# Optimization experiments

Measured on AMD Instinct MI355X. Metric: run time of the kernel, lower is better.

Reference implementation:

```python
import jax, jax.numpy as jnp
import numpy as np

N = 40000      # num atoms
E = 640000     # num edges (avg degree 16)
H = 128        # hidden_channels
R = 64         # num_rbf
NB = 3         # num interaction blocks
CUT = 5.0      # cutoff_upper
NT = 100       # num atom types (embedding rows)


def setup_inputs() -> dict:
    key = jax.random.key(0)
    ks = jax.random.split(key, 24)

    def lin_w(k, fan_in, fan_out):
        # xavier-uniform-like scale
        lim = np.sqrt(6.0 / (fan_in + fan_out)).astype(np.float32)
        return jax.random.uniform(k, (fan_in, fan_out), jnp.float32, -lim, lim)

    def stack_w(k, fan_in, fan_out):
        kk = jax.random.split(k, NB)
        return jnp.stack([lin_w(kk[i], fan_in, fan_out) for i in range(NB)])

    inp = {}
    inp["atom_types"] = jax.random.randint(ks[0], (N,), 0, NT)
    inp["edge_index"] = jax.random.randint(ks[1], (2, E), 0, N)
    inp["edge_weight"] = jax.random.uniform(ks[2], (E,), jnp.float32) * CUT

    inp["emb"] = jax.random.normal(ks[3], (NT, H), jnp.float32) * 0.1
    # CFConv params per block (stacked on leading NB axis)
    inp["lin1_w"] = stack_w(ks[4], H, H)            # no bias
    inp["fw1"] = stack_w(ks[5], R, H)
    inp["fb1"] = jnp.zeros((NB, H), jnp.float32)
    inp["fw2"] = stack_w(ks[6], H, H)
    inp["fb2"] = jnp.zeros((NB, H), jnp.float32)
    inp["lin2_w"] = stack_w(ks[7], H, H)
    inp["lin2_b"] = jnp.zeros((NB, H), jnp.float32)
    # InteractionBlock trailing linear
    inp["lin_w"] = stack_w(ks[8], H, H)
    inp["lin_b"] = jnp.zeros((NB, H), jnp.float32)
    # output network: H -> H//2 -> 1
    inp["o1_w"] = lin_w(ks[9], H, H // 2)
    inp["o1_b"] = jnp.zeros((H // 2,), jnp.float32)
    inp["o2_w"] = lin_w(ks[10], H // 2, 1)
    inp["o2_b"] = jnp.zeros((1,), jnp.float32)
    return inp


def _schnet_fwd(atom_types, edge_index, edge_weight, emb, lin1_w, fw1, fb1,
                fw2, fb2, lin2_w, lin2_b, lin_w, lin_b, o1_w, o1_b, o2_w, o2_b):
    # Gaussian RBF expansion of distances: (E, R)
    offsets = jnp.linspace(0.0, CUT, R).astype(edge_weight.dtype)
    coeff = -0.5 / (offsets[1] - offsets[0]) ** 2
    rbf = jnp.exp(coeff * (edge_weight[:, None] - offsets[None, :]) ** 2)
    # cosine cutoff envelope: (E,)
    C = 0.5 * (jnp.cos(jnp.pi * edge_weight / CUT) + 1.0)
    C = C * (edge_weight < CUT).astype(edge_weight.dtype)

    src = edge_index[0]
    dst = edge_index[1]

    x = emb[atom_types]  # (N, H)
    for b in range(NB):
        # filter network on expanded distances: (E, H)
        W = jnp.tanh(rbf @ fw1[b] + fb1[b]) @ fw2[b] + fb2[b]
        W = W * C[:, None]
        # CFConv: project, gather by src, modulate, scatter-sum to dst
        h = x @ lin1_w[b]                              # (N, H)
        msg = h[src] * W                               # (E, H)
        agg = jax.ops.segment_sum(msg, dst, num_segments=N)  # (N, H)
        y = agg @ lin2_w[b] + lin2_b[b]
        # InteractionBlock tail: activation then linear; residual in SchNet
        y = jnp.tanh(y) @ lin_w[b] + lin_b[b]
        x = x + y
    # output network: per-atom scalar energies (N, 1)
    energy = jnp.tanh(x @ o1_w + o1_b) @ o2_w + o2_b
    return energy


def reference(atom_types, edge_index, edge_weight, emb, lin1_w, fw1, fb1,
              fw2, fb2, lin2_w, lin2_b, lin_w, lin_b, o1_w, o1_b, o2_w, o2_b):
    return _schnet_fwd(atom_types, edge_index, edge_weight, emb, lin1_w, fw1,
                       fb1, fw2, fb2, lin2_w, lin2_b, lin_w, lin_b, o1_w,
                       o1_b, o2_w, o2_b)
```

## Files before the change

### kernel.cpp

```cpp
#include <hip/hip_runtime.h>
#include <math.h>

#define N_ATOMS 40000
#define E_EDGES 640000
#define H 128
#define RBF 64
#define NBLK 3
#define CUTF 5.0f
#define TBL 4096

__device__ __forceinline__ float fast_tanh(float x) {
    return 1.0f - 2.0f / (1.0f + __expf(2.0f * x));
}

__global__ __launch_bounds__(128) void k_embw(const float* __restrict__ emb,
                                              const float* __restrict__ lin1,
                                              float* __restrict__ embw) {
    const int t = blockIdx.x;
    const int c = threadIdx.x;
    float s = 0.0f;
#pragma unroll 8
    for (int k = 0; k < H; ++k) s = fmaf(emb[t * H + k], lin1[(size_t)k * H + c], s);
    embw[t * H + c] = s;
}

__global__ __launch_bounds__(256) void k_embed2(const int* __restrict__ types,
                                                const float* __restrict__ emb,
                                                const float* __restrict__ embw,
                                                float* __restrict__ x,
                                                float* __restrict__ h) {
    int flat4 = blockIdx.x * 256 + threadIdx.x;
    int i = flat4 >> 5;
    int c4 = flat4 & 31;
    int t = types[i];
    ((float4*)(x + (size_t)i * H))[c4] = ((const float4*)(emb + (size_t)t * H))[c4];
    ((float4*)(h + (size_t)i * H))[c4] = ((const float4*)(embw + (size_t)t * H))[c4];
}

__global__ __launch_bounds__(256) void k_count(const int* __restrict__ eidx,
                                               int* __restrict__ cnt) {
    int e = blockIdx.x * 256 + threadIdx.x;
    atomicAdd(&cnt[eidx[E_EDGES + e]], 1);
}

__global__ __launch_bounds__(1024) void k_scanA(const int* __restrict__ cnt,
                                                int* __restrict__ bsum) {
    __shared__ int ws[16];
    const int tid = threadIdx.x, lane = tid & 63, wid = tid >> 6;
    int idx = blockIdx.x * 1024 + tid;
    int v = (idx < N_ATOMS) ? cnt[idx] : 0;
#pragma unroll
    for (int off = 32; off; off >>= 1) v += __shfl_xor(v, off, 64);
    if (lane == 0) ws[wid] = v;
    __syncthreads();
    if (tid == 0) {
        int s = 0;
#pragma unroll
        for (int w = 0; w < 16; ++w) s += ws[w];
        bsum[blockIdx.x] = s;
    }
}

__global__ __launch_bounds__(64) void k_scanB(const int* __restrict__ bsum,
                                              int* __restrict__ boff) {
    const int lane = threadIdx.x;
    int v = (lane < 40) ? bsum[lane] : 0;
    int inc = v;
#pragma unroll
    for (int off = 1; off < 64; off <<= 1) {
        int t = __shfl_up(inc, off, 64);
        if (lane >= off) inc += t;
    }
    if (lane < 40) boff[lane] = inc - v;
}

__global__ __launch_bounds__(1024) void k_scanC(const int* __restrict__ cnt,
                                                const int* __restrict__ boff,
                                                int* __restrict__ cursor,
                                                int* __restrict__ rstart) {
    __shared__ int wsum[16];
    __shared__ int woff[16];
    const int tid = threadIdx.x, lane = tid & 63, wid = tid >> 6;
    int idx = blockIdx.x * 1024 + tid;
    int v = (idx < N_ATOMS) ? cnt[idx] : 0;
    int inc = v;
#pragma unroll
    for (int off = 1; off < 64; off <<= 1) {
        int t = __shfl_up(inc, off, 64);
        if (lane >= off) inc += t;
    }
    if (lane == 63) wsum[wid] = inc;
    __syncthreads();
    if (tid == 0) {
        int acc = 0;
#pragma unroll
        for (int w = 0; w < 16; ++w) { woff[w] = acc; acc += wsum[w]; }
    }
    __syncthreads();
    if (idx < N_ATOMS) {
        int ex = boff[blockIdx.x] + woff[wid] + inc - v;
        cursor[idx] = ex;
        rstart[idx] = ex;
    }
}

__global__ __launch_bounds__(256) void k_fill(const int* __restrict__ eidx,
                                              const float* __restrict__ ew,
                                              int* __restrict__ cursor,
                                              int2* __restrict__ pmeta) {
    int e = blockIdx.x * 256 + threadIdx.x;
    int dd = eidx[E_EDGES + e];
    int pos = atomicAdd(&cursor[dd], 1);
    float u = ew[e] * ((float)(TBL - 1) / CUTF);
    pmeta[pos] = make_int2(eidx[e], __float_as_int(u));
}

__global__ __launch_bounds__(256, 2) void k_table(const float* __restrict__ fw1all,
                                                  const float* __restrict__ fb1all,
                                                  const float* __restrict__ fw2all,
                                                  const float* __restrict__ fb2all,
                                                  float* __restrict__ tab) {
    const int b = blockIdx.y;
    const float* fw1 = fw1all + (size_t)b * RBF * H;
    const float* fb1 = fb1all + (size_t)b * H;
    const float* fw2 = fw2all + (size_t)b * H * H;
    const float* fb2 = fb2all + (size_t)b * H;
    float* tabB = tab + (size_t)b * TBL * H;

    __shared__ float tile[128 * 133];
    const int tid = threadIdx.x;
    const int mbase = blockIdx.x * 128;
    const float DSTEP = CUTF / (float)(TBL - 1);

    {
        const int e = tid & 127;
        const int k0 = (tid >> 7) * 32;
        const float d = (float)(mbase + e) * DSTEP;
        const float DELTA = CUTF / 63.0f;
        const float COEFF = -0.5f / (DELTA * DELTA);
#pragma unroll
        for (int k = k0; k < k0 + 32; ++k) {
            float diff = d - (float)k * DELTA;
            tile[e * 133 + k] = __expf(COEFF * diff * diff);
        }
    }
    __syncthreads();

    const int eg = tid >> 4, cg = tid & 15;
    const int e0 = eg * 8, c0 = cg * 8;

    float acc[8][8];
#pragma unroll
    for (int i = 0; i < 8; ++i)
#pragma unroll
        for (int j = 0; j < 8; ++j) acc[i][j] = 0.0f;

#pragma unroll 4
    for (int k = 0; k < RBF; ++k) {
        float a[8];
#pragma unroll
        for (int i = 0; i < 8; ++i) a[i] = tile[(e0 + i) * 133 + k];
        const float4 b0 = *(const float4*)(fw1 + (size_t)k * H + c0);
        const float4 b1 = *(const float4*)(fw1 + (size_t)k * H + c0 + 4);
        const float bb[8] = {b0.x, b0.y, b0.z, b0.w, b1.x, b1.y, b1.z, b1.w};
#pragma unroll
        for (int i = 0; i < 8; ++i)
#pragma unroll
            for (int j = 0; j < 8; ++j) acc[i][j] = fmaf(a[i], bb[j], acc[i][j]);
    }

    {
        const float4 q0 = *(const float4*)(fb1 + c0);
        const float4 q1 = *(const float4*)(fb1 + c0 + 4);
        const float bv[8] = {q0.x, q0.y, q0.z, q0.w, q1.x, q1.y, q1.z, q1.w};
#pragma unroll
        for (int i = 0; i < 8; ++i)
#pragma unroll
            for (int j = 0; j < 8; ++j) acc[i][j] = fast_tanh(acc[i][j] + bv[j]);
    }

    __syncthreads();
#pragma unroll
    for (int i = 0; i < 8; ++i)
#pragma unroll
        for (int j = 0; j < 8; ++j) tile[(e0 + i) * 133 + c0 + j] = acc[i][j];
    __syncthreads();

#pragma unroll
    for (int i = 0; i < 8; ++i)
#pragma unroll
        for (int j = 0; j < 8; ++j) acc[i][j] = 0.0f;

#pragma unroll 4
    for (int k = 0; k < H; ++k) {
        float a[8];
#pragma unroll
        for (int i = 0; i < 8; ++i) a[i] = tile[(e0 + i) * 133 + k];
        const float4 b0 = *(const float4*)(fw2 + (size_t)k * H + c0);
        const float4 b1 = *(const float4*)(fw2 + (size_t)k * H + c0 + 4);
        const float bb[8] = {b0.x, b0.y, b0.z, b0.w, b1.x, b1.y, b1.z, b1.w};
#pragma unroll
        for (int i = 0; i < 8; ++i)
#pragma unroll
            for (int j = 0; j < 8; ++j) acc[i][j] = fmaf(a[i], bb[j], acc[i][j]);
    }

    const float4 q0 = *(const float4*)(fb2 + c0);
    const float4 q1 = *(const float4*)(fb2 + c0 + 4);
    const float bv[8] = {q0.x, q0.y, q0.z, q0.w, q1.x, q1.y, q1.z, q1.w};

#pragma unroll
    for (int ei = 0; ei < 8; ++ei) {
        const int m = mbase + e0 + ei;
        const float d = (float)m * DSTEP;
        float c = 0.5f * (cosf(0.6283185307179586f * d) + 1.0f);
        c = (d < CUTF) ? c : 0.0f;
        float* op = tabB + (size_t)m * H + c0;
        float r[8];
#pragma unroll
        for (int j = 0; j < 8; ++j) r[j] = (acc[ei][j] + bv[j]) * c;
        *(float4*)(op)     = make_float4(r[0], r[1], r[2], r[3]);
        *(float4*)(op + 4) = make_float4(r[4], r[5], r[6], r[7]);
    }
}

__device__ __forceinline__ void gemm_pipe(const float* __restrict__ at,
                                          const float* __restrict__ W,
                                          int r0, int c0, float acc[4][8]) {
#pragma unroll
    for (int i = 0; i < 4; ++i)
#pragma unroll
        for (int j = 0; j < 8; ++j) acc[i][j] = 0.0f;

    const float* Wc = W + c0;
    float4 a0l = *(const float4*)(Wc);
    float4 a0h = *(const float4*)(Wc + 4);
    float4 a1l = *(const float4*)(Wc + H);
    float4 a1h = *(const float4*)(Wc + H + 4);

#pragma unroll 2
    for (int k = 0; k < H; k += 4) {
        float4 b0l = *(const float4*)(Wc + (size_t)(k + 2) * H);
        float4 b0h = *(const float4*)(Wc + (size_t)(k + 2) * H + 4);
        float4 b1l = *(const float4*)(Wc + (size_t)(k + 3) * H);
        float4 b1h = *(const float4*)(Wc + (size_t)(k + 3) * H + 4);
        {
            float a[4], b[4];
#pragma unroll
            for (int i = 0; i < 4; ++i) {
                a[i] = at[(r0 + i) * 133 + k];
                b[i] = at[(r0 + i) * 133 + k + 1];
            }
            const float w0[8] = {a0l.x, a0l.y, a0l.z, a0l.w, a0h.x, a0h.y, a0h.z, a0h.w};
            const float w1[8] = {a1l.x, a1l.y, a1l.z, a1l.w, a1h.x, a1h.y, a1h.z, a1h.w};
#pragma unroll
            for (int i = 0; i < 4; ++i)
#pragma unroll
                for (int j = 0; j < 8; ++j) acc[i][j] = fmaf(a[i], w0[j], acc[i][j]);
#pragma unroll
            for (int i = 0; i < 4; ++i)
#pragma unroll
                for (int j = 0; j < 8; ++j) acc[i][j] = fmaf(b[i], w1[j], acc[i][j]);
        }
        const int kn = (k + 4) & (H - 1);
        a0l = *(const float4*)(Wc + (size_t)kn * H);
        a0h = *(const float4*)(Wc + (size_t)kn * H + 4);
        a1l = *(const float4*)(Wc + (size_t)(kn + 1) * H);
        a1h = *(const float4*)(Wc + (size_t)(kn + 1) * H + 4);
        {
            float a[4], b[4];
#pragma unroll
            for (int i = 0; i < 4; ++i) {
                a[i] = at[(r0 + i) * 133 + k + 2];
                b[i] = at[(r0 + i) * 133 + k + 3];
            }
            const float w0[8] = {b0l.x, b0l.y, b0l.z, b0l.w, b0h.x, b0h.y, b0h.z, b0h.w};
            const float w1[8] = {b1l.x, b1l.y, b1l.z, b1l.w, b1h.x, b1h.y, b1h.z, b1h.w};
#pragma unroll
            for (int i = 0; i < 4; ++i)
#pragma unroll
                for (int j = 0; j < 8; ++j) acc[i][j] = fmaf(a[i], w0[j], acc[i][j]);
#pragma unroll
            for (int i = 0; i < 4; ++i)
#pragma unroll
                for (int j = 0; j < 8; ++j) acc[i][j] = fmaf(b[i], w1[j], acc[i][j]);
        }
    }
}

template <bool MAKE_H>
__global__ __launch_bounds__(256) void k_tail(const float* __restrict__ agg,
                                              const float* __restrict__ lin2,
                                              const float* __restrict__ b2,
                                              const float* __restrict__ linw,
                                              const float* __restrict__ bl,
                                              float* __restrict__ x,
                                              const float* __restrict__ lin1n,
                                              float* __restrict__ hout) {
    __shared__ float at[64 * 133];
    const int tid = threadIdx.x;
    const int abase = blockIdx.x * 64;

#pragma unroll
    for (int i = 0; i < 8; ++i) {
        int flat4 = tid + 256 * i;
        int r = flat4 >> 5, k4 = flat4 & 31;
        float4 v = ((const float4*)(agg + (size_t)(abase + r) * H))[k4];
        float* dp = &at[r * 133 + k4 * 4];
        dp[0] = v.x; dp[1] = v.y; dp[2] = v.z; dp[3] = v.w;
    }
    __syncthreads();

    const int eg = tid >> 4, cg = tid & 15;
    const int r0 = eg * 4, c0 = cg * 8;

    float acc[4][8];

    gemm_pipe(at, lin2, r0, c0, acc);
    {
        const float4 q0 = *(const float4*)(b2 + c0);
        const float4 q1 = *(const float4*)(b2 + c0 + 4);
        const float bv[8] = {q0.x, q0.y, q0.z, q0.w, q1.x, q1.y, q1.z, q1.w};
#pragma unroll
        for (int i = 0; i < 4; ++i)
#pragma unroll
            for (int j = 0; j < 8; ++j) acc[i][j] = fast_tanh(acc[i][j] + bv[j]);
    }

    __syncthreads();
#pragma unroll
    for (int i = 0; i < 4; ++i)
#pragma unroll
        for (int j = 0; j < 8; ++j) at[(r0 + i) * 133 + c0 + j] = acc[i][j];
    __syncthreads();

    gemm_pipe(at, linw, r0, c0, acc);
    {
        const float4 q0 = *(const float4*)(bl + c0);
        const float4 q1 = *(const float4*)(bl + c0 + 4);
        const float bv[8] = {q0.x, q0.y, q0.z, q0.w, q1.x, q1.y, q1.z, q1.w};
        if (MAKE_H) __syncthreads();
#pragma unroll
        for (int ei = 0; ei < 4; ++ei) {
            const int row = abase + r0 + ei;
            float* op = x + (size_t)row * H + c0;
            float4 x0 = *(const float4*)(op);
            float4 x1 = *(const float4*)(op + 4);
            float xn[8] = {x0.x + acc[ei][0] + bv[0], x0.y + acc[ei][1] + bv[1],
                           x0.z + acc[ei][2] + bv[2], x0.w + acc[ei][3] + bv[3],
                           x1.x + acc[ei][4] + bv[4], x1.y + acc[ei][5] + bv[5],
                           x1.z + acc[ei][6] + bv[6], x1.w + acc[ei][7] + bv[7]};
            *(float4*)(op)     = make_float4(xn[0], xn[1], xn[2], xn[3]);
            *(float4*)(op + 4) = make_float4(xn[4], xn[5], xn[6], xn[7]);
            if (MAKE_H) {
#pragma unroll
                for (int j = 0; j < 8; ++j) at[(r0 + ei) * 133 + c0 + j] = xn[j];
            }
        }
    }

    if (MAKE_H) {
        __syncthreads();
        gemm_pipe(at, lin1n, r0, c0, acc);
#pragma unroll
        for (int ei = 0; ei < 4; ++ei) {
            const int row = abase + r0 + ei;
            float* op = hout + (size_t)row * H + c0;
            *(float4*)(op)     = make_float4(acc[ei][0], acc[ei][1], acc[ei][2], acc[ei][3]);
            *(float4*)(op + 4) = make_float4(acc[ei][4], acc[ei][5], acc[ei][6], acc[ei][7]);
        }
    }
}

__global__ __launch_bounds__(256) void k_edge4(const int* __restrict__ rstart,
                                               const int* __restrict__ rend,
                                               const int2* __restrict__ pmeta,
                                               const float* __restrict__ tab,
                                               const float* __restrict__ h,
                                               float* __restrict__ agg) {
    const int wave = threadIdx.x >> 6;
    const int lane = threadIdx.x & 63;
    const int a = blockIdx.x * 4 + wave;
    const int col0 = lane * 2;

    const int s = rstart[a];
    const int n = rend[a] - s;

    float s0 = 0.0f, s1 = 0.0f;
    if (n <= 64) {
        int2 meta = make_int2(0, 0);
        if (lane < n) meta = pmeta[s + lane];
#pragma unroll 2
        for (int e = 0; e < n; ++e) {
            const int src = __shfl(meta.x, e, 64);
            const float u = __int_as_float(__shfl(meta.y, e, 64));
            int i0 = (int)u;
            i0 = (i0 > TBL - 2) ? (TBL - 2) : i0;
            const float f = u - (float)i0;
            const float2 lo = *(const float2*)(tab + (size_t)i0 * H + col0);
            const float2 hi = *(const float2*)(tab + ((size_t)i0 + 1) * H + col0);
            const float2 hv = *(const float2*)(h + (size_t)src * H + col0);
            s0 = fmaf(fmaf(f, hi.x - lo.x, lo.x), hv.x, s0);
            s1 = fmaf(fmaf(f, hi.y - lo.y, lo.y), hv.y, s1);
        }
    } else {
        for (int e = s; e < s + n; ++e) {
            const int2 m = pmeta[e];
            const float u = __int_as_float(m.y);
            int i0 = (int)u;
            i0 = (i0 > TBL - 2) ? (TBL - 2) : i0;
            const float f = u - (float)i0;
            const float2 lo = *(const float2*)(tab + (size_t)i0 * H + col0);
            const float2 hi = *(const float2*)(tab + ((size_t)i0 + 1) * H + col0);
            const float2 hv = *(const float2*)(h + (size_t)m.x * H + col0);
            s0 = fmaf(fmaf(f, hi.x - lo.x, lo.x), hv.x, s0);
            s1 = fmaf(fmaf(f, hi.y - lo.y, lo.y), hv.y, s1);
        }
    }
    *(float2*)(agg + (size_t)a * H + col0) = make_float2(s0, s1);
}

__global__ __launch_bounds__(256) void k_out(const float* __restrict__ x,
                                             const float* __restrict__ o1w,
                                             const float* __restrict__ o1b,
                                             const float* __restrict__ o2w,
                                             const float* __restrict__ o2b,
                                             float* __restrict__ out) {
    __shared__ float xs[64 * 132];
    const int tid = threadIdx.x;
    const int abase = blockIdx.x * 64;

#pragma unroll
    for (int i = 0; i < 8; ++i) {
        int flat4 = tid + 256 * i;
        int r = flat4 >> 5, k4 = flat4 & 31;
        float4 v = ((const float4*)(x + (size_t)(abase + r) * H))[k4];
        float* dp = &xs[r * 132 + k4 * 4];
        dp[0] = v.x; dp[1] = v.y; dp[2] = v.z; dp[3] = v.w;
    }
    __syncthreads();

    const int eg = tid >> 4, cg = tid & 15;
    const int r0 = eg * 4, c0 = cg * 4;

    float acc[4][4];
#pragma unroll
    for (int i = 0; i < 4; ++i)
#pragma unroll
        for (int j = 0; j < 4; ++j) acc[i][j] = 0.0f;

#pragma unroll 4
    for (int k = 0; k < H; ++k) {
        float a[4];
#pragma unroll
        for (int i = 0; i < 4; ++i) a[i] = xs[(r0 + i) * 132 + k];
        const float4 b = *(const float4*)(o1w + (size_t)k * 64 + c0);
        const float bb[4] = {b.x, b.y, b.z, b.w};
#pragma unroll
        for (int i = 0; i < 4; ++i)
#pragma unroll
            for (int j = 0; j < 4; ++j) acc[i][j] = fmaf(a[i], bb[j], acc[i][j]);
    }

    const float4 ob = *(const float4*)(o1b + c0);
    const float4 ow = *(const float4*)(o2w + c0);
    const float obv[4] = {ob.x, ob.y, ob.z, ob.w};
    const float owv[4] = {ow.x, ow.y, ow.z, ow.w};
    float p[4];
#pragma unroll
    for (int i = 0; i < 4; ++i) {
        float s = 0.0f;
#pragma unroll
        for (int j = 0; j < 4; ++j) s = fmaf(fast_tanh(acc[i][j] + obv[j]), owv[j], s);
        p[i] = s;
    }
#pragma unroll
    for (int off = 1; off < 16; off <<= 1) {
#pragma unroll
        for (int i = 0; i < 4; ++i) p[i] += __shfl_xor(p[i], off, 64);
    }
    if (cg == 0) {
        const float b2 = o2b[0];
#pragma unroll
        for (int i = 0; i < 4; ++i) out[abase + r0 + i] = p[i] + b2;
    }
}

extern "C" void kernel_launch(void* const* d_in, const int* in_sizes, int n_in,
                              void* d_out, int out_size, void* d_ws, size_t ws_size,
                              hipStream_t stream) {
    const int*   types = (const int*)d_in[0];
    const int*   eidx  = (const int*)d_in[1];
    const float* ew    = (const float*)d_in[2];
    const float* emb   = (const float*)d_in[3];
    const float* lin1  = (const float*)d_in[4];
    const float* fw1   = (const float*)d_in[5];
    const float* fb1   = (const float*)d_in[6];
    const float* fw2   = (const float*)d_in[7];
    const float* fb2   = (const float*)d_in[8];
    const float* lin2  = (const float*)d_in[9];
    const float* lin2b = (const float*)d_in[10];
    const float* linw  = (const float*)d_in[11];
    const float* linb  = (const float*)d_in[12];
    const float* o1w   = (const float*)d_in[13];
    const float* o1b   = (const float*)d_in[14];
    const float* o2w   = (const float*)d_in[15];
    const float* o2b   = (const float*)d_in[16];
    float* out = (float*)d_out;

    float* x      = (float*)d_ws;
    float* h      = x + (size_t)N_ATOMS * H;
    float* agg    = h + (size_t)N_ATOMS * H;
    float* tab    = agg + (size_t)N_ATOMS * H;
    float* embw   = tab + (size_t)NBLK * TBL * H;
    int*   cnt    = (int*)(embw + 100 * H);
    int*   cursor = cnt + N_ATOMS;
    int*   rstart = cursor + N_ATOMS;
    int*   bsum   = rstart + N_ATOMS;
    int*   boff   = bsum + 64;
    int2*  pmeta  = (int2*)(boff + 64);

    hipMemsetAsync(cnt, 0, N_ATOMS * sizeof(int), stream);
    k_count<<<E_EDGES / 256, 256, 0, stream>>>(eidx, cnt);
    k_scanA<<<40, 1024, 0, stream>>>(cnt, bsum);
    k_scanB<<<1, 64, 0, stream>>>(bsum, boff);
    k_scanC<<<40, 1024, 0, stream>>>(cnt, boff, cursor, rstart);
    k_fill<<<E_EDGES / 256, 256, 0, stream>>>(eidx, ew, cursor, pmeta);

    k_embw<<<100, 128, 0, stream>>>(emb, lin1, embw);
    k_embed2<<<(N_ATOMS * H / 4) / 256, 256, 0, stream>>>(types, emb, embw, x, h);
    k_table<<<dim3(TBL / 128, NBLK), 256, 0, stream>>>(fw1, fb1, fw2, fb2, tab);

    for (int b = 0; b < NBLK; ++b) {
        k_edge4<<<N_ATOMS / 4, 256, 0, stream>>>(rstart, cursor, pmeta,
                                                 tab + (size_t)b * TBL * H, h, agg);
        if (b < NBLK - 1) {
            k_tail<true><<<N_ATOMS / 64, 256, 0, stream>>>(
                agg, lin2 + (size_t)b * H * H, lin2b + (size_t)b * H,
                linw + (size_t)b * H * H, linb + (size_t)b * H, x,
                lin1 + (size_t)(b + 1) * H * H, h);
        } else {
            k_tail<false><<<N_ATOMS / 64, 256, 0, stream>>>(
                agg, lin2 + (size_t)b * H * H, lin2b + (size_t)b * H,
                linw + (size_t)b * H * H, linb + (size_t)b * H, x,
                nullptr, nullptr);
        }
    }

    k_out<<<N_ATOMS / 64, 256, 0, stream>>>(x, o1w, o1b, o2w, o2b, out);
}
```

Before: 642.9 us.

## Stage weight panels into LDS with async global_load_lds double buffering in tail GEMM

Replaces the per-thread global weight loads in the tail kernel's 64x128x128 GEMMs with 32-row weight panels copied into shared memory through global_load_lds, double-buffered so the next panel loads while the current one is used. The activation tile pitch changes from 133 to 132 so rows can be read as float4. The aim is to cut redundant global/L2 traffic for the weights and issue fewer, wider LDS reads. In exchange the block uses about 32KB more LDS, which may lower occupancy, and the 132 pitch may cause LDS bank conflicts. Removing some barriers leans on the syncs inside gemm_lds, and the staged panels depend on async LDS writes being complete before __syncthreads.

```diff
diff --git a/kernel.cpp b/kernel.cpp
--- a/kernel.cpp
+++ b/kernel.cpp
@@ -224,67 +224,59 @@
     }
 }
 
-__device__ __forceinline__ void gemm_pipe(const float* __restrict__ at,
-                                          const float* __restrict__ W,
-                                          int r0, int c0, float acc[4][8]) {
+__device__ __forceinline__ void stage_panel(const float* __restrict__ Wg,
+                                            float* wbuf, int tid) {
+    const int w = tid >> 6, lane = tid & 63;
+#pragma unroll
+    for (int i = 0; i < 4; ++i) {
+        const float* g = Wg + ((w << 2) + i) * 256 + (lane << 2);
+        float* l = wbuf + ((w << 2) + i) * 256;
+        __builtin_amdgcn_global_load_lds((const __attribute__((address_space(1))) void*)g,
+                                         (__attribute__((address_space(3))) void*)l,
+                                         16, 0, 0);
+    }
+}
+
+__device__ __forceinline__ void gemm_lds(const float* __restrict__ at,
+                                         const float* __restrict__ Wg,
+                                         float* __restrict__ wb0,
+                                         float* __restrict__ wb1,
+                                         int tid, int r0, int c0, float acc[4][8]) {
 #pragma unroll
     for (int i = 0; i < 4; ++i)
 #pragma unroll
         for (int j = 0; j < 8; ++j) acc[i][j] = 0.0f;
 
-    const float* Wc = W + c0;
-    float4 a0l = *(const float4*)(Wc);
-    float4 a0h = *(const float4*)(Wc + 4);
-    float4 a1l = *(const float4*)(Wc + H);
-    float4 a1h = *(const float4*)(Wc + H + 4);
-
-#pragma unroll 2
-    for (int k = 0; k < H; k += 4) {
-        float4 b0l = *(const float4*)(Wc + (size_t)(k + 2) * H);
-        float4 b0h = *(const float4*)(Wc + (size_t)(k + 2) * H + 4);
-        float4 b1l = *(const float4*)(Wc + (size_t)(k + 3) * H);
-        float4 b1h = *(const float4*)(Wc + (size_t)(k + 3) * H + 4);
-        {
-            float a[4], b[4];
-#pragma unroll
-            for (int i = 0; i < 4; ++i) {
-                a[i] = at[(r0 + i) * 133 + k];
-                b[i] = at[(r0 + i) * 133 + k + 1];
+    stage_panel(Wg, wb0, tid);
+    __syncthreads();
+
+#pragma unroll
+    for (int p = 0; p < 4; ++p) {
+        float* cur = (p & 1) ? wb1 : wb0;
+        float* nxt = (p & 1) ? wb0 : wb1;
+        if (p < 3) stage_panel(Wg + (size_t)(p + 1) * 32 * H, nxt, tid);
+        const int kb = p * 32;
+#pragma unroll
+        for (int k4 = 0; k4 < 32; k4 += 4) {
+            float4 av[4];
+#pragma unroll
+            for (int i = 0; i < 4; ++i)
+                av[i] = *(const float4*)&at[(r0 + i) * 132 + kb + k4];
+            const float* avf = (const float*)av;
+#pragma unroll
+            for (int kk = 0; kk < 4; ++kk) {
+                const float4 w0 = *(const float4*)&cur[(k4 + kk) * H + c0];
+                const float4 w1 = *(const float4*)&cur[(k4 + kk) * H + c0 + 4];
+                const float wv[8] = {w0.x, w0.y, w0.z, w0.w, w1.x, w1.y, w1.z, w1.w};
+#pragma unroll
+                for (int i = 0; i < 4; ++i) {
+                    const float a = avf[i * 4 + kk];
+#pragma unroll
+                    for (int j = 0; j < 8; ++j) acc[i][j] = fmaf(a, wv[j], acc[i][j]);
+                }
             }
-            const float w0[8] = {a0l.x, a0l.y, a0l.z, a0l.w, a0h.x, a0h.y, a0h.z, a0h.w};
-            const float w1[8] = {a1l.x, a1l.y, a1l.z, a1l.w, a1h.x, a1h.y, a1h.z, a1h.w};
-#pragma unroll
-            for (int i = 0; i < 4; ++i)
-#pragma unroll
-                for (int j = 0; j < 8; ++j) acc[i][j] = fmaf(a[i], w0[j], acc[i][j]);
-#pragma unroll
-            for (int i = 0; i < 4; ++i)
-#pragma unroll
-                for (int j = 0; j < 8; ++j) acc[i][j] = fmaf(b[i], w1[j], acc[i][j]);
-        }
-        const int kn = (k + 4) & (H - 1);
-        a0l = *(const float4*)(Wc + (size_t)kn * H);
-        a0h = *(const float4*)(Wc + (size_t)kn * H + 4);
-        a1l = *(const float4*)(Wc + (size_t)(kn + 1) * H);
-        a1h = *(const float4*)(Wc + (size_t)(kn + 1) * H + 4);
-        {
-            float a[4], b[4];
-#pragma unroll
-            for (int i = 0; i < 4; ++i) {
-                a[i] = at[(r0 + i) * 133 + k + 2];
-                b[i] = at[(r0 + i) * 133 + k + 3];
-            }
-            const float w0[8] = {b0l.x, b0l.y, b0l.z, b0l.w, b0h.x, b0h.y, b0h.z, b0h.w};
-            const float w1[8] = {b1l.x, b1l.y, b1l.z, b1l.w, b1h.x, b1h.y, b1h.z, b1h.w};
-#pragma unroll
-            for (int i = 0; i < 4; ++i)
-#pragma unroll
-                for (int j = 0; j < 8; ++j) acc[i][j] = fmaf(a[i], w0[j], acc[i][j]);
-#pragma unroll
-            for (int i = 0; i < 4; ++i)
-#pragma unroll
-                for (int j = 0; j < 8; ++j) acc[i][j] = fmaf(b[i], w1[j], acc[i][j]);
-        }
+        }
+        __syncthreads();
     }
 }
 
@@ -297,7 +289,9 @@
                                               float* __restrict__ x,
                                               const float* __restrict__ lin1n,
                                               float* __restrict__ hout) {
-    __shared__ float at[64 * 133];
+    __shared__ float at[64 * 132];
+    __shared__ float wpan0[32 * H];
+    __shared__ float wpan1[32 * H];
     const int tid = threadIdx.x;
     const int abase = blockIdx.x * 64;
 
@@ -306,17 +300,15 @@
         int flat4 = tid + 256 * i;
         int r = flat4 >> 5, k4 = flat4 & 31;
         float4 v = ((const float4*)(agg + (size_t)(abase + r) * H))[k4];
-        float* dp = &at[r * 133 + k4 * 4];
-        dp[0] = v.x; dp[1] = v.y; dp[2] = v.z; dp[3] = v.w;
-    }
-    __syncthreads();
+        *(float4*)&at[r * 132 + k4 * 4] = v;
+    }
 
     const int eg = tid >> 4, cg = tid & 15;
     const int r0 = eg * 4, c0 = cg * 8;
 
     float acc[4][8];
 
-    gemm_pipe(at, lin2, r0, c0, acc);
+    gemm_lds(at, lin2, wpan0, wpan1, tid, r0, c0, acc);
     {
         const float4 q0 = *(const float4*)(b2 + c0);
         const float4 q1 = *(const float4*)(b2 + c0 + 4);
@@ -326,20 +318,17 @@
 #pragma unroll
             for (int j = 0; j < 8; ++j) acc[i][j] = fast_tanh(acc[i][j] + bv[j]);
     }
-
-    __syncthreads();
 #pragma unroll
     for (int i = 0; i < 4; ++i)
 #pragma unroll
-        for (int j = 0; j < 8; ++j) at[(r0 + i) * 133 + c0 + j] = acc[i][j];
-    __syncthreads();
-
-    gemm_pipe(at, linw, r0, c0, acc);
+        for (int j = 0; j < 8; ++j) at[(r0 + i) * 132 + c0 + j] = acc[i][j];
+    __syncthreads();
+
+    gemm_lds(at, linw, wpan0, wpan1, tid, r0, c0, acc);
     {
         const float4 q0 = *(const float4*)(bl + c0);
         const float4 q1 = *(const float4*)(bl + c0 + 4);
         const float bv[8] = {q0.x, q0.y, q0.z, q0.w, q1.x, q1.y, q1.z, q1.w};
-        if (MAKE_H) __syncthreads();
 #pragma unroll
         for (int ei = 0; ei < 4; ++ei) {
             const int row = abase + r0 + ei;
@@ -354,14 +343,14 @@
             *(float4*)(op + 4) = make_float4(xn[4], xn[5], xn[6], xn[7]);
             if (MAKE_H) {
 #pragma unroll
-                for (int j = 0; j < 8; ++j) at[(r0 + ei) * 133 + c0 + j] = xn[j];
+                for (int j = 0; j < 8; ++j) at[(r0 + ei) * 132 + c0 + j] = xn[j];
             }
         }
     }
 
     if (MAKE_H) {
         __syncthreads();
-        gemm_pipe(at, lin1n, r0, c0, acc);
+        gemm_lds(at, lin1n, wpan0, wpan1, tid, r0, c0, acc);
 #pragma unroll
         for (int ei = 0; ei < 4; ++ei) {
             const int row = abase + r0 + ei;
```

Result: no change. 638.4 us (-0.7%).
